# Kernel tuning notes

Hardware: AMD Instinct MI355X
Metric: run time of the kernel (lower is better)

The kernel has to match this reference:

```python
import jax, jax.numpy as jnp
import numpy as np

INPUT_DIM = 1024
OUTPUT_DIM = 1024
DEGREE = 8


def setup_inputs() -> dict:
    key = jax.random.key(0)
    k1, k2 = jax.random.split(key)
    x = jax.random.normal(k1, (8192, INPUT_DIM), dtype=jnp.float32)
    std = 1.0 / (INPUT_DIM * (DEGREE + 1))
    cheby_coeffs = jax.random.normal(k2, (INPUT_DIM, OUTPUT_DIM, DEGREE + 1), dtype=jnp.float32) * std
    return {"x": x, "cheby_coeffs": cheby_coeffs}


def reference(x, cheby_coeffs):
    # x: [B, I]; cheby_coeffs: [I, O, D+1]
    degree = cheby_coeffs.shape[-1] - 1
    t = jnp.clip(jnp.tanh(x), -0.999, 0.999)            # [B, I]
    theta = jnp.arccos(t)[..., None]                     # [B, I, 1]
    arange = jnp.arange(degree + 1, dtype=x.dtype)       # [D+1]
    basis = jnp.cos(theta * arange)                      # [B, I, D+1] Chebyshev T_d(t)
    y = jnp.einsum('bid,iod->bo', basis, cheby_coeffs)   # [B, O]
    return y
```

## Files before the change

kernel.cpp:

```cpp
#include <hip/hip_runtime.h>
#include <stdint.h>

#define B_ROWS 8192
#define I_DIM  1024
#define N_DIM  1024
#define NDEG   9
#define K_DIM  (I_DIM * (NDEG-1))

#define BM 256
#define BN 128
#define BK 64
#define NT (K_DIM / BK)

typedef __attribute__((ext_vector_type(8)))  short short8;
typedef __attribute__((ext_vector_type(16))) float f32x16;

__device__ __forceinline__ unsigned short f2bf(float f) {
  union { float f; uint32_t u; } v; v.f = f;
  uint32_t u = v.u;
  u += 0x7FFFu + ((u >> 16) & 1u);
  return (unsigned short)(u >> 16);
}

__device__ __forceinline__ float bf2f(unsigned short h) {
  union { uint32_t u; float f; } v; v.u = ((uint32_t)h) << 16;
  return v.f;
}

__device__ __forceinline__ int h2(int r) { return (r >> 2) & 7; }

__global__ __launch_bounds__(256) void prep_kernel(const float* __restrict__ x,
                                                   const float* __restrict__ cf,
                                                   unsigned short* __restrict__ A,
                                                   unsigned short* __restrict__ Bt,
                                                   float* __restrict__ bias,
                                                   int repack_blocks) {
  __shared__ unsigned short L[32][584];
  const int tid = threadIdx.x;

  if ((int)blockIdx.x < repack_blocks) {
    const int bx = blockIdx.x;
    const int i0 = (bx & 31) * 32;
    const int o0 = (bx >> 5) * 64;

    #pragma unroll
    for (int j = 0; j < 18; ++j) {
      const int f4  = j * 256 + tid;
      const int il  = f4 / 144;
      const int odq = f4 % 144;
      const float4 v = *reinterpret_cast<const float4*>(
          cf + ((size_t)(i0 + il) * N_DIM + o0) * NDEG + (size_t)odq * 4);
      ushort4 w;
      w.x = f2bf(v.x); w.y = f2bf(v.y); w.z = f2bf(v.z); w.w = f2bf(v.w);
      *reinterpret_cast<ushort4*>(&L[il][odq * 4]) = w;
    }
    __syncthreads();

    for (int od = tid; od < 576; od += 256) {
      const int o = od / 9, d = od % 9;
      if (d == 0) {
        float s = 0.f;
        #pragma unroll
        for (int il = 0; il < 32; ++il) s += bf2f(L[il][od]);
        atomicAdd(&bias[o0 + o], s);
      } else {
        const size_t base = (size_t)(o0 + o) * K_DIM + (size_t)(d - 1) * I_DIM + i0;
        #pragma unroll
        for (int ci = 0; ci < 4; ++ci) {
          uint32_t uu[4];
          #pragma unroll
          for (int p = 0; p < 4; ++p) {
            unsigned short lo = L[ci * 8 + p * 2 + 0][od];
            unsigned short hi = L[ci * 8 + p * 2 + 1][od];
            uu[p] = (uint32_t)lo | ((uint32_t)hi << 16);
          }
          uint4 u; u.x = uu[0]; u.y = uu[1]; u.z = uu[2]; u.w = uu[3];
          *reinterpret_cast<uint4*>(Bt + base + ci * 8) = u;
        }
      }
    }
  } else {
    const int b  = blockIdx.x - repack_blocks;
    const int i0 = tid * 4;
    const float4 xv = *reinterpret_cast<const float4*>(x + (size_t)b * I_DIM + i0);
    float t[4];
    t[0] = fminf(fmaxf(tanhf(xv.x), -0.999f), 0.999f);
    t[1] = fminf(fmaxf(tanhf(xv.y), -0.999f), 0.999f);
    t[2] = fminf(fmaxf(tanhf(xv.z), -0.999f), 0.999f);
    t[3] = fminf(fmaxf(tanhf(xv.w), -0.999f), 0.999f);

    unsigned short* outb = A + (size_t)b * K_DIM + i0;
    float Tp[4] = {1.f, 1.f, 1.f, 1.f};
    float Tc[4] = {t[0], t[1], t[2], t[3]};
    #pragma unroll
    for (int d = 1; d < NDEG; ++d) {
      ushort4 o4;
      o4.x = f2bf(Tc[0]); o4.y = f2bf(Tc[1]); o4.z = f2bf(Tc[2]); o4.w = f2bf(Tc[3]);
      *reinterpret_cast<ushort4*>(outb + (size_t)(d - 1) * I_DIM) = o4;
      if (d < NDEG - 1) {
        #pragma unroll
        for (int j = 0; j < 4; ++j) {
          float Tn = 2.0f * t[j] * Tc[j] - Tp[j];
          Tp[j] = Tc[j]; Tc[j] = Tn;
        }
      }
    }
  }
}

__global__ __launch_bounds__(512, 2) void gemm_kernel(const unsigned short* __restrict__ A,
                                                      const unsigned short* __restrict__ Bt,
                                                      const float* __restrict__ bias,
                                                      float* __restrict__ C) {
  extern __shared__ unsigned short sm[];
  const int tid  = threadIdx.x;
  const int lane = tid & 63;
  const int wave = tid >> 6;
  const int l31  = lane & 31;
  const int half = lane >> 5;
  const int wm   = wave >> 1;
  const int wn   = wave & 1;
  const int m0   = blockIdx.x * BM;
  const int n0   = blockIdx.y * BN;

  const int sr   = tid >> 3;
  const int slot = tid & 7;

  const unsigned short* Abase = A  + (size_t)m0 * K_DIM;
  const unsigned short* Bbase = Bt + (size_t)n0 * K_DIM;

  f32x16 acc[2][2];
  #pragma unroll
  for (int a = 0; a < 2; ++a)
    #pragma unroll
    for (int b = 0; b < 2; ++b)
      #pragma unroll
      for (int r = 0; r < 16; ++r)
        acc[a][b][r] = 0.f;

#define STAGE_A(s, bf, kk) { const int r_ = (s)*64 + sr; const int gc_ = slot ^ h2(r_);     \
    __builtin_amdgcn_global_load_lds(                                                       \
        (const __attribute__((address_space(1))) void*)(Abase + (size_t)r_*K_DIM + (kk) + gc_*8), \
        (__attribute__((address_space(3))) void*)&sm[(bf)*16384 + r_*64 + slot*8], 16, 0, 0); }
#define STAGE_B(s, bf, kk) { const int r_ = (s)*64 + sr; const int gc_ = slot ^ h2(r_);     \
    __builtin_amdgcn_global_load_lds(                                                       \
        (const __attribute__((address_space(1))) void*)(Bbase + (size_t)r_*K_DIM + (kk) + gc_*8), \
        (__attribute__((address_space(3))) void*)&sm[49152 + (bf)*8192 + r_*64 + slot*8], 16, 0, 0); }
#define STAGE6(bf, kk) { STAGE_A(0, bf, kk) STAGE_A(1, bf, kk) STAGE_A(2, bf, kk) STAGE_A(3, bf, kk) \
                         STAGE_B(0, bf, kk) STAGE_B(1, bf, kk) }

  STAGE6(0, 0)
  STAGE6(1, BK)
  asm volatile("s_waitcnt vmcnt(6)" ::: "memory");
  __builtin_amdgcn_s_barrier();

  const int rowA0 = wm * 64 + l31;
  const int rowA1 = wm * 64 + 32 + l31;
  const int rowB0 = wn * 64 + l31;
  const int rowB1 = wn * 64 + 32 + l31;

  int cur = 0;
  for (int kt = 0; kt < NT; ++kt) {
    const unsigned short* Asc = &sm[cur * 16384];
    const unsigned short* Bsc = &sm[49152 + cur * 8192];
    const int s2 = (cur == 0) ? 2 : cur - 1;

    short8 av[2][4], bv[2][4];
    #pragma unroll
    for (int ks = 0; ks < 4; ++ks) {
      const int c = ks * 2 + half;
      av[0][ks] = *reinterpret_cast<const short8*>(&Asc[rowA0 * 64 + (c ^ h2(rowA0)) * 8]);
      av[1][ks] = *reinterpret_cast<const short8*>(&Asc[rowA1 * 64 + (c ^ h2(rowA1)) * 8]);
      bv[0][ks] = *reinterpret_cast<const short8*>(&Bsc[rowB0 * 64 + (c ^ h2(rowB0)) * 8]);
      bv[1][ks] = *reinterpret_cast<const short8*>(&Bsc[rowB1 * 64 + (c ^ h2(rowB1)) * 8]);
    }

    if (kt + 2 < NT) { STAGE6(s2, (kt + 2) * BK) }

    __builtin_amdgcn_s_setprio(1);
    #pragma unroll
    for (int ks = 0; ks < 4; ++ks) {
      acc[0][0] = __builtin_amdgcn_mfma_f32_32x32x16_bf16(av[0][ks], bv[0][ks], acc[0][0], 0, 0, 0);
      acc[0][1] = __builtin_amdgcn_mfma_f32_32x32x16_bf16(av[0][ks], bv[1][ks], acc[0][1], 0, 0, 0);
      acc[1][0] = __builtin_amdgcn_mfma_f32_32x32x16_bf16(av[1][ks], bv[0][ks], acc[1][0], 0, 0, 0);
      acc[1][1] = __builtin_amdgcn_mfma_f32_32x32x16_bf16(av[1][ks], bv[1][ks], acc[1][1], 0, 0, 0);
    }
    __builtin_amdgcn_s_setprio(0);

    if (kt < NT - 1) {
      if (kt < NT - 2) asm volatile("s_waitcnt vmcnt(6)" ::: "memory");
      else             asm volatile("s_waitcnt vmcnt(0)" ::: "memory");
      __builtin_amdgcn_s_barrier();
    }
    cur = (cur == 2) ? 0 : cur + 1;
  }
#undef STAGE_A
#undef STAGE_B
#undef STAGE6

  #pragma unroll
  for (int ni = 0; ni < 2; ++ni) {
    const int col  = n0 + wn * 64 + ni * 32 + l31;
    const float bc = bias[col];
    #pragma unroll
    for (int mi = 0; mi < 2; ++mi) {
      const int rbase = m0 + wm * 64 + mi * 32 + 4 * half;
      #pragma unroll
      for (int r = 0; r < 16; ++r) {
        const int row = rbase + (r & 3) + 8 * (r >> 2);
        C[(size_t)row * N_DIM + col] = acc[mi][ni][r] + bc;
      }
    }
  }
}

extern "C" void kernel_launch(void* const* d_in, const int* in_sizes, int n_in,
                              void* d_out, int out_size, void* d_ws, size_t ws_size,
                              hipStream_t stream) {
  const float* x      = (const float*)d_in[0];
  const float* coeffs = (const float*)d_in[1];
  float* y            = (float*)d_out;

  const size_t bt_bytes = (size_t)N_DIM * K_DIM * sizeof(unsigned short);
  unsigned short* Bt = (unsigned short*)d_ws;
  float* bias        = (float*)((char*)d_ws + bt_bytes);
  unsigned short* A  = (unsigned short*)((char*)d_ws + bt_bytes + 4096);

  hipMemsetAsync(bias, 0, N_DIM * sizeof(float), stream);

  hipFuncSetAttribute((const void*)gemm_kernel,
                      hipFuncAttributeMaxDynamicSharedMemorySize, 147456);

  size_t avail    = (ws_size > bt_bytes + 4096) ? (ws_size - bt_bytes - 4096) : 0;
  size_t rows_fit = avail / ((size_t)K_DIM * sizeof(unsigned short));
  int m_chunk = (int)((rows_fit / BM) * BM);
  if (m_chunk > B_ROWS) m_chunk = B_ROWS;
  if (m_chunk < BM)     m_chunk = BM;

  for (int m0 = 0; m0 < B_ROWS; m0 += m_chunk) {
    int mc = B_ROWS - m0; if (mc > m_chunk) mc = m_chunk;
    const int rb = (m0 == 0) ? 512 : 0;
    prep_kernel<<<rb + mc, 256, 0, stream>>>(x + (size_t)m0 * I_DIM, coeffs, A, Bt, bias, rb);
    gemm_kernel<<<dim3(mc / BM, N_DIM / BN), 512, 147456, stream>>>(
        A, Bt, bias, y + (size_t)m0 * N_DIM);
  }
}
```

Before: 286.6 us.

## Switch GEMM to double-buffered LDS with interleaved reads, and speed up prep

The GEMM main loop moves from a 3-stage LDS ring to a 2-stage double buffer. It issues the next tile's global-to-LDS loads first, then interleaves the LDS reads for each k-step with the MFMAs using sched_group_barrier hints, and drops the setprio calls. This shrinks LDS use from 147456 to 98304 bytes, but it now waits vmcnt(0) every iteration, which exposes more load latency. The prep kernel separately switches to an exp-based fast tanh and processes 8 elements per thread with two rows per block, halving its grid.

```diff
diff --git a/kernel.cpp b/kernel.cpp
--- a/kernel.cpp
+++ b/kernel.cpp
@@ -25,6 +25,11 @@
 __device__ __forceinline__ float bf2f(unsigned short h) {
   union { uint32_t u; float f; } v; v.u = ((uint32_t)h) << 16;
   return v.f;
+}
+
+__device__ __forceinline__ float fast_tanh(float x) {
+  float e = __expf(2.0f * x);
+  return 1.0f - __fdividef(2.0f, e + 1.0f);
 }
 
 __device__ __forceinline__ int h2(int r) { return (r >> 2) & 7; }
@@ -80,28 +85,34 @@
       }
     }
   } else {
-    const int b  = blockIdx.x - repack_blocks;
-    const int i0 = tid * 4;
-    const float4 xv = *reinterpret_cast<const float4*>(x + (size_t)b * I_DIM + i0);
-    float t[4];
-    t[0] = fminf(fmaxf(tanhf(xv.x), -0.999f), 0.999f);
-    t[1] = fminf(fmaxf(tanhf(xv.y), -0.999f), 0.999f);
-    t[2] = fminf(fmaxf(tanhf(xv.z), -0.999f), 0.999f);
-    t[3] = fminf(fmaxf(tanhf(xv.w), -0.999f), 0.999f);
+    const int b  = ((int)blockIdx.x - repack_blocks) * 2 + (tid >> 7);
+    const int j  = tid & 127;
+    const int i0 = j * 8;
+    const float4 xv0 = *reinterpret_cast<const float4*>(x + (size_t)b * I_DIM + i0);
+    const float4 xv1 = *reinterpret_cast<const float4*>(x + (size_t)b * I_DIM + i0 + 4);
+    float t[8];
+    t[0] = fast_tanh(xv0.x); t[1] = fast_tanh(xv0.y);
+    t[2] = fast_tanh(xv0.z); t[3] = fast_tanh(xv0.w);
+    t[4] = fast_tanh(xv1.x); t[5] = fast_tanh(xv1.y);
+    t[6] = fast_tanh(xv1.z); t[7] = fast_tanh(xv1.w);
+    #pragma unroll
+    for (int p = 0; p < 8; ++p) t[p] = fminf(fmaxf(t[p], -0.999f), 0.999f);
 
     unsigned short* outb = A + (size_t)b * K_DIM + i0;
-    float Tp[4] = {1.f, 1.f, 1.f, 1.f};
-    float Tc[4] = {t[0], t[1], t[2], t[3]};
+    float Tp[8], Tc[8];
+    #pragma unroll
+    for (int p = 0; p < 8; ++p) { Tp[p] = 1.f; Tc[p] = t[p]; }
     #pragma unroll
     for (int d = 1; d < NDEG; ++d) {
-      ushort4 o4;
-      o4.x = f2bf(Tc[0]); o4.y = f2bf(Tc[1]); o4.z = f2bf(Tc[2]); o4.w = f2bf(Tc[3]);
-      *reinterpret_cast<ushort4*>(outb + (size_t)(d - 1) * I_DIM) = o4;
+      short8 o;
+      #pragma unroll
+      for (int p = 0; p < 8; ++p) o[p] = (short)f2bf(Tc[p]);
+      *reinterpret_cast<short8*>(outb + (size_t)(d - 1) * I_DIM) = o;
       if (d < NDEG - 1) {
         #pragma unroll
-        for (int j = 0; j < 4; ++j) {
-          float Tn = 2.0f * t[j] * Tc[j] - Tp[j];
-          Tp[j] = Tc[j]; Tc[j] = Tn;
+        for (int p = 0; p < 8; ++p) {
+          float Tn = 2.0f * t[p] * Tc[p] - Tp[p];
+          Tp[p] = Tc[p]; Tc[p] = Tn;
         }
       }
     }
@@ -145,54 +156,55 @@
 #define STAGE_B(s, bf, kk) { const int r_ = (s)*64 + sr; const int gc_ = slot ^ h2(r_);     \
     __builtin_amdgcn_global_load_lds(                                                       \
         (const __attribute__((address_space(1))) void*)(Bbase + (size_t)r_*K_DIM + (kk) + gc_*8), \
-        (__attribute__((address_space(3))) void*)&sm[49152 + (bf)*8192 + r_*64 + slot*8], 16, 0, 0); }
+        (__attribute__((address_space(3))) void*)&sm[32768 + (bf)*8192 + r_*64 + slot*8], 16, 0, 0); }
 #define STAGE6(bf, kk) { STAGE_A(0, bf, kk) STAGE_A(1, bf, kk) STAGE_A(2, bf, kk) STAGE_A(3, bf, kk) \
                          STAGE_B(0, bf, kk) STAGE_B(1, bf, kk) }
-
-  STAGE6(0, 0)
-  STAGE6(1, BK)
-  asm volatile("s_waitcnt vmcnt(6)" ::: "memory");
-  __builtin_amdgcn_s_barrier();
 
   const int rowA0 = wm * 64 + l31;
   const int rowA1 = wm * 64 + 32 + l31;
   const int rowB0 = wn * 64 + l31;
   const int rowB1 = wn * 64 + 32 + l31;
-
-  int cur = 0;
+  const int hA0 = h2(rowA0), hA1 = h2(rowA1), hB0 = h2(rowB0), hB1 = h2(rowB1);
+
+  STAGE6(0, 0)
+  asm volatile("s_waitcnt vmcnt(0)" ::: "memory");
+  __builtin_amdgcn_s_barrier();
+
   for (int kt = 0; kt < NT; ++kt) {
+    const int  cur  = kt & 1;
+    const int  nxt  = cur ^ 1;
+    const bool more = (kt + 1 < NT);
     const unsigned short* Asc = &sm[cur * 16384];
-    const unsigned short* Bsc = &sm[49152 + cur * 8192];
-    const int s2 = (cur == 0) ? 2 : cur - 1;
+    const unsigned short* Bsc = &sm[32768 + cur * 8192];
+
+    if (more) { STAGE6(nxt, (kt + 1) * BK) }
+    __builtin_amdgcn_sched_barrier(0);
 
     short8 av[2][4], bv[2][4];
+#define READ4(ks) {                                                                          \
+    const int c_ = (ks) * 2 + half;                                                          \
+    av[0][ks] = *reinterpret_cast<const short8*>(&Asc[rowA0 * 64 + (c_ ^ hA0) * 8]);         \
+    av[1][ks] = *reinterpret_cast<const short8*>(&Asc[rowA1 * 64 + (c_ ^ hA1) * 8]);         \
+    bv[0][ks] = *reinterpret_cast<const short8*>(&Bsc[rowB0 * 64 + (c_ ^ hB0) * 8]);         \
+    bv[1][ks] = *reinterpret_cast<const short8*>(&Bsc[rowB1 * 64 + (c_ ^ hB1) * 8]); }
+
+    READ4(0)
     #pragma unroll
     for (int ks = 0; ks < 4; ++ks) {
-      const int c = ks * 2 + half;
-      av[0][ks] = *reinterpret_cast<const short8*>(&Asc[rowA0 * 64 + (c ^ h2(rowA0)) * 8]);
-      av[1][ks] = *reinterpret_cast<const short8*>(&Asc[rowA1 * 64 + (c ^ h2(rowA1)) * 8]);
-      bv[0][ks] = *reinterpret_cast<const short8*>(&Bsc[rowB0 * 64 + (c ^ h2(rowB0)) * 8]);
-      bv[1][ks] = *reinterpret_cast<const short8*>(&Bsc[rowB1 * 64 + (c ^ h2(rowB1)) * 8]);
-    }
-
-    if (kt + 2 < NT) { STAGE6(s2, (kt + 2) * BK) }
-
-    __builtin_amdgcn_s_setprio(1);
-    #pragma unroll
-    for (int ks = 0; ks < 4; ++ks) {
+      if (ks < 3) READ4(ks + 1)
       acc[0][0] = __builtin_amdgcn_mfma_f32_32x32x16_bf16(av[0][ks], bv[0][ks], acc[0][0], 0, 0, 0);
       acc[0][1] = __builtin_amdgcn_mfma_f32_32x32x16_bf16(av[0][ks], bv[1][ks], acc[0][1], 0, 0, 0);
       acc[1][0] = __builtin_amdgcn_mfma_f32_32x32x16_bf16(av[1][ks], bv[0][ks], acc[1][0], 0, 0, 0);
       acc[1][1] = __builtin_amdgcn_mfma_f32_32x32x16_bf16(av[1][ks], bv[1][ks], acc[1][1], 0, 0, 0);
-    }
-    __builtin_amdgcn_s_setprio(0);
-
-    if (kt < NT - 1) {
-      if (kt < NT - 2) asm volatile("s_waitcnt vmcnt(6)" ::: "memory");
-      else             asm volatile("s_waitcnt vmcnt(0)" ::: "memory");
+      if (ks < 3) __builtin_amdgcn_sched_group_barrier(0x100, 4, 0);
+      __builtin_amdgcn_sched_group_barrier(0x008, 4, 0);
+    }
+#undef READ4
+
+    if (more) {
+      asm volatile("s_waitcnt vmcnt(0)" ::: "memory");
       __builtin_amdgcn_s_barrier();
     }
-    cur = (cur == 2) ? 0 : cur + 1;
   }
 #undef STAGE_A
 #undef STAGE_B
@@ -229,7 +241,7 @@
   hipMemsetAsync(bias, 0, N_DIM * sizeof(float), stream);
 
   hipFuncSetAttribute((const void*)gemm_kernel,
-                      hipFuncAttributeMaxDynamicSharedMemorySize, 147456);
+                      hipFuncAttributeMaxDynamicSharedMemorySize, 98304);
 
   size_t avail    = (ws_size > bt_bytes + 4096) ? (ws_size - bt_bytes - 4096) : 0;
   size_t rows_fit = avail / ((size_t)K_DIM * sizeof(unsigned short));
@@ -240,8 +252,8 @@
   for (int m0 = 0; m0 < B_ROWS; m0 += m_chunk) {
     int mc = B_ROWS - m0; if (mc > m_chunk) mc = m_chunk;
     const int rb = (m0 == 0) ? 512 : 0;
-    prep_kernel<<<rb + mc, 256, 0, stream>>>(x + (size_t)m0 * I_DIM, coeffs, A, Bt, bias, rb);
-    gemm_kernel<<<dim3(mc / BM, N_DIM / BN), 512, 147456, stream>>>(
+    prep_kernel<<<rb + mc / 2, 256, 0, stream>>>(x + (size_t)m0 * I_DIM, coeffs, A, Bt, bias, rb);
+    gemm_kernel<<<dim3(mc / BM, N_DIM / BN), 512, 98304, stream>>>(
         A, Bt, bias, y + (size_t)m0 * N_DIM);
   }
 }
```

After: 263.9 us. -7.9%, faster.
